# Optimization experiments

Measured on AMD Instinct MI355X. Metric: run time of the kernel, lower is better.

## Reference

```python
import jax, jax.numpy as jnp
import numpy as np

B, C, H, W = 16, 256, 56, 56
NH = 8           # num_heads
BS = 8           # block_size
HALO = 3         # halo_size
WIN = BS + 2 * HALO   # 14
MLP = 4


def setup_inputs() -> dict:
    key = jax.random.key(0)
    ks = jax.random.split(key, 8)
    f = lambda k, shape, s: jax.random.normal(k, shape, jnp.float32) * s
    return dict(
        x=jax.random.normal(ks[0], (B, C, H, W), jnp.float32),
        ln1_g=jnp.ones((C,), jnp.float32), ln1_b=jnp.zeros((C,), jnp.float32),
        wq=f(ks[1], (C, C), C ** -0.5), bq=jnp.zeros((C,), jnp.float32),
        wkv=f(ks[2], (2 * C, C), C ** -0.5), bkv=jnp.zeros((2 * C,), jnp.float32),
        bias=f(ks[3], (1, NH, 1, BS * BS, WIN * WIN), 0.02),
        gamma1=jnp.full((1, C, 1, 1), 1e-6, jnp.float32),
        ln2_g=jnp.ones((C,), jnp.float32), ln2_b=jnp.zeros((C,), jnp.float32),
        w1=f(ks[4], (MLP * C, C), 0.02), b1=jnp.zeros((MLP * C,), jnp.float32),
        w2=f(ks[5], (C, MLP * C), 0.02), b2=jnp.zeros((C,), jnp.float32),
        gamma2=jnp.full((1, 1, 1, C), 1e-6, jnp.float32),
    )


def _ln2d(x, g, b, eps=1e-5):
    # LayerNorm over channel dim of NCHW
    mu = jnp.mean(x, axis=1, keepdims=True)
    var = jnp.mean((x - mu) ** 2, axis=1, keepdims=True)
    return (x - mu) * jax.lax.rsqrt(var + eps) * g[None, :, None, None] + b[None, :, None, None]


def _halo_attn(x, wq, bq, wkv, bkv, bias):
    Bn, Cc, Hh, Ww = x.shape
    dh = Cc // NH
    scale = dh ** -0.5
    nHb, nWb = Hh // BS, Ww // BS
    xh = jnp.transpose(x, (0, 2, 3, 1))            # B,H,W,C
    q = xh @ wq.T + bq                             # 1x1 conv
    kv = xh @ wkv.T + bkv                          # B,H,W,2C
    # q blocks: B,nh,nblocks,bs^2,dh
    q = q.reshape(Bn, nHb, BS, nWb, BS, NH, dh).transpose(0, 5, 1, 3, 2, 4, 6)
    q = q.reshape(Bn, NH, nHb * nWb, BS * BS, dh)
    # kv halo windows
    kvp = jnp.pad(kv, ((0, 0), (HALO, HALO), (HALO, HALO), (0, 0)))
    ih = (jnp.arange(nHb) * BS)[:, None] + jnp.arange(WIN)[None, :]
    iw = (jnp.arange(nWb) * BS)[:, None] + jnp.arange(WIN)[None, :]
    kvw = kvp[:, ih[:, None, :, None], iw[None, :, None, :], :]
    kvw = kvw.reshape(Bn, nHb * nWb, WIN * WIN, NH, 2 * dh).transpose(0, 3, 1, 2, 4)
    k, v = kvw[..., :dh], kvw[..., dh:]
    attn = jnp.einsum('bhnqd,bhnkd->bhnqk', q, k) * scale + bias
    attn = jax.nn.softmax(attn, axis=-1)
    out = jnp.einsum('bhnqk,bhnkd->bhnqd', attn, v)                   # B,nh,nb,bs^2,dh
    out = out.reshape(Bn, NH, nHb, nWb, BS, BS, dh).transpose(0, 1, 6, 2, 4, 3, 5)
    return out.reshape(Bn, Cc, Hh, Ww)


def _forward(x, ln1_g, ln1_b, wq, bq, wkv, bkv, bias, gamma1,
             ln2_g, ln2_b, w1, b1, w2, b2, gamma2):
    shortcut = x
    a = _halo_attn(_ln2d(x, ln1_g, ln1_b), wq, bq, wkv, bkv, bias)
    x = shortcut + gamma1 * a
    shortcut = x
    y = jnp.transpose(_ln2d(x, ln2_g, ln2_b), (0, 2, 3, 1))           # NHWC
    y = jax.nn.gelu(y @ w1.T + b1, approximate=False) @ w2.T + b2
    y = gamma2 * y
    return shortcut + jnp.transpose(y, (0, 3, 1, 2))


def reference(x, ln1_g, ln1_b, wq, bq, wkv, bkv, bias, gamma1,
              ln2_g, ln2_b, w1, b1, w2, b2, gamma2):
    return _forward(x, ln1_g, ln1_b, wq, bq, wkv, bkv, bias, gamma1,
                    ln2_g, ln2_b, w1, b1, w2, b2, gamma2)
```

## Files before the change

### kernel.cpp

```cpp
#include <hip/hip_runtime.h>
#include <hip/hip_bf16.h>
#include <math.h>

typedef unsigned short u16;
typedef float f32x4 __attribute__((ext_vector_type(4)));
typedef __bf16 bf16x8 __attribute__((ext_vector_type(8)));

__device__ __forceinline__ float bf2f(u16 u) {
    union { float f; unsigned int i; } v; v.i = ((unsigned int)u) << 16; return v.f;
}
__device__ __forceinline__ u16 f2bf(float f) {
    union { float f; unsigned int i; } v; v.f = f;
    unsigned int x = v.i;
    return (u16)((x + 0x7FFFu + ((x >> 16) & 1u)) >> 16);
}
__device__ __forceinline__ unsigned int cvt_pk_bf16(float lo, float hi) {
    unsigned int r;
    asm("v_cvt_pk_bf16_f32 %0, %1, %2" : "=v"(r) : "v"(lo), "v"(hi));
    return r;
}

__global__ __launch_bounds__(256) void k_prep(const float* __restrict__ wq, const float* __restrict__ wkv,
                                              const float* __restrict__ w1, const float* __restrict__ w2,
                                              u16* __restrict__ wqkvb, u16* __restrict__ w1p, u16* __restrict__ w2p) {
    const int bid = blockIdx.x, t = threadIdx.x;
    if (bid < 192) {
        int e = (bid * 256 + t) * 4;
        const float* src = (e < 65536) ? (wq + e) : (wkv + (e - 65536));
        float sc = (e < 65536) ? 0.17677669529663687f : 1.f;
        float4 v = *(const float4*)src;
        ushort4 o;
        o.x = f2bf(v.x * sc); o.y = f2bf(v.y * sc); o.z = f2bf(v.z * sc); o.w = f2bf(v.w * sc);
        *(ushort4*)(wqkvb + e) = o;
    } else if (bid < 320) {
        int tid = (bid - 192) * 256 + t;
        int kc = tid >> 11, rem = tid & 2047;
        int wave = rem >> 9, rem2 = rem & 511;
        int ks = rem2 >> 6, lane = rem2 & 63;
        int ln = lane & 15, quad = lane >> 4;
        const float* src = w1 + (size_t)(kc * 64 + wave * 16 + ln) * 256 + ks * 32 + quad * 8;
        float4 v0 = *(const float4*)src;
        float4 v1 = *(const float4*)(src + 4);
        alignas(16) u16 tmp[8];
        tmp[0] = f2bf(v0.x); tmp[1] = f2bf(v0.y); tmp[2] = f2bf(v0.z); tmp[3] = f2bf(v0.w);
        tmp[4] = f2bf(v1.x); tmp[5] = f2bf(v1.y); tmp[6] = f2bf(v1.z); tmp[7] = f2bf(v1.w);
        *(int4*)(w1p + (size_t)tid * 8) = *(int4*)tmp;
    } else {
        int tid = (bid - 320) * 256 + t;
        int kc = tid >> 11, rem = tid & 2047;
        int wave = rem >> 9, rem2 = rem & 511;
        int ks2 = rem2 >> 8, rem3 = rem2 & 255;
        int nt = rem3 >> 6, lane = rem3 & 63;
        int ln = lane & 15, quad = lane >> 4;
        const float* src = w2 + (size_t)(wave * 64 + nt * 16 + ln) * 1024 + kc * 64 + ks2 * 32 + quad * 8;
        float4 v0 = *(const float4*)src;
        float4 v1 = *(const float4*)(src + 4);
        alignas(16) u16 tmp[8];
        tmp[0] = f2bf(v0.x); tmp[1] = f2bf(v0.y); tmp[2] = f2bf(v0.z); tmp[3] = f2bf(v0.w);
        tmp[4] = f2bf(v1.x); tmp[5] = f2bf(v1.y); tmp[6] = f2bf(v1.z); tmp[7] = f2bf(v1.w);
        *(int4*)(w2p + (size_t)tid * 8) = *(int4*)tmp;
    }
}

__global__ __launch_bounds__(256) void k_transpose(const float* __restrict__ x, u16* __restrict__ xh) {
    __shared__ __align__(16) u16 tile[64][72];
    const int t = threadIdx.x;
    const int hw0 = blockIdx.x * 64;
    const int c0  = blockIdx.y * 64;
    const int b   = blockIdx.z;
    const int cl = t >> 2, wl = (t & 3) * 16;
    {
        int c = c0 + cl;
        const float* src = x + (size_t)(b * 256 + c) * 3136 + hw0 + wl;
        for (int q = 0; q < 4; q++) {
            float4 v = *(const float4*)(src + q * 4);
            uint2 pr;
            pr.x = cvt_pk_bf16(v.x, v.y);
            pr.y = cvt_pk_bf16(v.z, v.w);
            *(uint2*)&tile[cl][wl + q * 4] = pr;
        }
    }
    __syncthreads();
    const int hl = t >> 3, cl2 = (t & 7) * 8;
    for (int i = 0; i < 2; i++) {
        int hw = hl + i * 32;
        alignas(16) u16 tmp[8];
        for (int j = 0; j < 8; j++) tmp[j] = tile[cl2 + j][hw];
        u16* dst = xh + (size_t)(b * 3136 + hw0 + hw) * 256 + c0 + cl2;
        *(int4*)dst = *(int4*)tmp;
    }
}

__global__ __launch_bounds__(256) void k_ln(const u16* __restrict__ in, u16* __restrict__ out,
                                            const float* __restrict__ g, const float* __restrict__ bta) {
    const int wave = threadIdx.x >> 6, lane = threadIdx.x & 63;
    const int p = blockIdx.x * 4 + wave;
    ushort4 v = *(const ushort4*)(in + (size_t)p * 256 + lane * 4);
    float f0 = bf2f(v.x), f1 = bf2f(v.y), f2 = bf2f(v.z), f3 = bf2f(v.w);
    float s = f0 + f1 + f2 + f3;
    float sq = f0 * f0 + f1 * f1 + f2 * f2 + f3 * f3;
    for (int o = 32; o >= 1; o >>= 1) { s += __shfl_xor(s, o, 64); sq += __shfl_xor(sq, o, 64); }
    float m = s * (1.f / 256.f);
    float var = sq * (1.f / 256.f) - m * m;
    float inv = rsqrtf(var + 1e-5f);
    float4 gv = *(const float4*)(g + lane * 4);
    float4 bv = *(const float4*)(bta + lane * 4);
    uint2 o2;
    o2.x = cvt_pk_bf16((f0 - m) * inv * gv.x + bv.x, (f1 - m) * inv * gv.y + bv.y);
    o2.y = cvt_pk_bf16((f2 - m) * inv * gv.z + bv.z, (f3 - m) * inv * gv.w + bv.w);
    *(uint2*)(out + (size_t)p * 256 + lane * 4) = o2;
}

__global__ __launch_bounds__(256) void k_qkv(
    const u16* __restrict__ xn, const u16* __restrict__ Bw,
    const float* __restrict__ bq, const float* __restrict__ bkv,
    u16* __restrict__ out) {
    __shared__ __align__(16) u16 smem[17408];
    u16* As = smem;
    u16* Bs = smem + 4096;

    const int g = blockIdx.x;
    const int xcd = g & 7, idx = g >> 3;
    const int bm = xcd * 49 + idx / 6, bn = idx % 6;

    const int t = threadIdx.x;
    const int wave = t >> 6, lane = t & 63;
    const int wm = (wave >> 1) * 64, wn = (wave & 1) * 64;
    const int ln = lane & 15, quad = lane >> 4;

    f32x4 vzero = {0.f, 0.f, 0.f, 0.f};
    f32x4 acc[4][4];
    for (int i = 0; i < 4; i++) for (int j = 0; j < 4; j++) acc[i][j] = vzero;

    const int srow = t >> 2;
    const int scol = (t & 3) * 8;

    for (int k0 = 0; k0 < 256; k0 += 32) {
        for (int i = 0; i < 2; i++) {
            int r = srow + i * 64;
            *(int4*)&As[r * 32 + scol] = *(const int4*)(xn + (size_t)(bm * 128 + r) * 256 + k0 + scol);
            *(int4*)&Bs[r * 32 + scol] = *(const int4*)(Bw + (size_t)(bn * 128 + r) * 256 + k0 + scol);
        }
        __syncthreads();
        bf16x8 af[4], bfr[4];
        for (int mt = 0; mt < 4; mt++) af[mt] = *(const bf16x8*)&As[(wm + mt * 16 + ln) * 32 + quad * 8];
        for (int nt = 0; nt < 4; nt++) bfr[nt] = *(const bf16x8*)&Bs[(wn + nt * 16 + ln) * 32 + quad * 8];
        for (int mt = 0; mt < 4; mt++)
            for (int nt = 0; nt < 4; nt++)
                acc[mt][nt] = __builtin_amdgcn_mfma_f32_16x16x32_bf16(bfr[nt], af[mt], acc[mt][nt], 0, 0, 0);
        __syncthreads();
    }

    u16* Cs = smem;
    for (int nt = 0; nt < 4; nt++) {
        int gn0 = bn * 128 + wn + nt * 16 + quad * 4;
        f32x4 bv;
        if (gn0 < 256) {
            f32x4 tq = *(const f32x4*)(bq + gn0);
            bv = tq * 0.17677669529663687f;
        } else {
            bv = *(const f32x4*)(bkv + gn0 - 256);
        }
        for (int mt = 0; mt < 4; mt++) {
            uint2 pk2;
            pk2.x = cvt_pk_bf16(acc[mt][nt][0] + bv[0], acc[mt][nt][1] + bv[1]);
            pk2.y = cvt_pk_bf16(acc[mt][nt][2] + bv[2], acc[mt][nt][3] + bv[3]);
            *(uint2*)&Cs[(wm + mt * 16 + ln) * 136 + wn + nt * 16 + quad * 4] = pk2;
        }
    }
    __syncthreads();
    const int row = t >> 4, col = (t & 15) * 8;
    for (int pass = 0; pass < 8; pass++) {
        int rr = pass * 16 + row;
        int4 v = *(int4*)&Cs[rr * 136 + col];
        *(int4*)(out + (size_t)(bm * 128 + rr) * 768 + bn * 128 + col) = v;
    }
}

__global__ __launch_bounds__(256) void k_mlp(
    const u16* __restrict__ xn, const u16* __restrict__ x2,
    const u16* __restrict__ w1p, const float* __restrict__ b1,
    const u16* __restrict__ w2p, const float* __restrict__ b2,
    const float* __restrict__ g2v, float* __restrict__ outT) {
    __shared__ __align__(16) u16 smem[16896 + 8704];
    u16* As = smem;
    u16* Hs = smem + 16896;

    const int g = blockIdx.x;
    const int bm = (g & 7) * 98 + (g >> 3);

    const int t = threadIdx.x;
    const int wave = t >> 6, lane = t & 63;
    const int ln = lane & 15, quad = lane >> 4;
    const int wn64 = wave * 64;
    const int wq4 = wave * 2;

    f32x4 vzero = {0.f, 0.f, 0.f, 0.f};
    f32x4 acc[4][4];
    for (int i = 0; i < 4; i++) for (int j = 0; j < 4; j++) acc[i][j] = vzero;

    {
        const int srow = t >> 2, scb = (t & 3) * 8;
        for (int c = 0; c < 8; c++) {
            int col = scb + c * 32;
            *(int4*)&As[srow * 264 + col] = *(const int4*)(xn + (size_t)(bm * 64 + srow) * 256 + col);
        }
    }
    __syncthreads();

    for (int kc = 0; kc < 8; kc++) {
        bf16x8 w1f[2][8];
        {
            const u16* w1b = w1p + (size_t)(kc * 8 + wq4) * 4096 + lane * 8;
            #pragma unroll
            for (int nt = 0; nt < 2; nt++)
                #pragma unroll
                for (int ks = 0; ks < 8; ks++)
                    w1f[nt][ks] = *(const bf16x8*)(w1b + nt * 4096 + ks * 512);
        }
        f32x4 up[4][2];
        #pragma unroll
        for (int i = 0; i < 4; i++) { up[i][0] = vzero; up[i][1] = vzero; }
        #pragma unroll
        for (int ks = 0; ks < 8; ks++) {
            #pragma unroll
            for (int mt = 0; mt < 4; mt++) {
                bf16x8 af = *(const bf16x8*)&As[(mt * 16 + ln) * 264 + ks * 32 + quad * 8];
                up[mt][0] = __builtin_amdgcn_mfma_f32_16x16x32_bf16(w1f[0][ks], af, up[mt][0], 0, 0, 0);
                up[mt][1] = __builtin_amdgcn_mfma_f32_16x16x32_bf16(w1f[1][ks], af, up[mt][1], 0, 0, 0);
            }
        }
        bf16x8 w2f[4][4];
        #pragma unroll
        for (int ks2 = 0; ks2 < 4; ks2++) {
            const u16* w2b = w2p + (size_t)((((kc * 2 + (ks2 >> 1)) * 4 + wave) * 2 + (ks2 & 1)) * 4) * 512 + lane * 8;
            #pragma unroll
            for (int nt = 0; nt < 4; nt++)
                w2f[ks2][nt] = *(const bf16x8*)(w2b + nt * 512);
        }
        __syncthreads();
        #pragma unroll
        for (int nt = 0; nt < 2; nt++) {
            float4 bv = *(const float4*)(b1 + kc * 128 + wave * 32 + nt * 16 + quad * 4);
            #pragma unroll
            for (int mt = 0; mt < 4; mt++) {
                float v0 = up[mt][nt][0] + bv.x;
                float v1 = up[mt][nt][1] + bv.y;
                float v2 = up[mt][nt][2] + bv.z;
                float v3 = up[mt][nt][3] + bv.w;
                uint2 pk;
                pk.x = cvt_pk_bf16(v0 * (1.f / (1.f + __expf(-1.702f * v0))),
                                   v1 * (1.f / (1.f + __expf(-1.702f * v1))));
                pk.y = cvt_pk_bf16(v2 * (1.f / (1.f + __expf(-1.702f * v2))),
                                   v3 * (1.f / (1.f + __expf(-1.702f * v3))));
                *(uint2*)&Hs[(mt * 16 + ln) * 136 + wave * 32 + nt * 16 + quad * 4] = pk;
            }
        }
        __syncthreads();
        #pragma unroll
        for (int ks2 = 0; ks2 < 4; ks2++) {
            bf16x8 hf[4];
            #pragma unroll
            for (int mt = 0; mt < 4; mt++)
                hf[mt] = *(const bf16x8*)&Hs[(mt * 16 + ln) * 136 + ks2 * 32 + quad * 8];
            #pragma unroll
            for (int nt = 0; nt < 4; nt++) {
                #pragma unroll
                for (int mt = 0; mt < 4; mt++)
                    acc[mt][nt] = __builtin_amdgcn_mfma_f32_16x16x32_bf16(hf[mt], w2f[ks2][nt], acc[mt][nt], 0, 0, 0);
            }
        }
    }

    const int b = bm / 49;
    for (int nt = 0; nt < 4; nt++) {
        int gn = wn64 + nt * 16 + ln;
        float bs = b2[gn], g2 = g2v[gn];
        for (int mt = 0; mt < 4; mt++) {
            int gm0 = bm * 64 + mt * 16 + quad * 4;
            int hw0 = gm0 - b * 3136;
            f32x4 res;
            for (int r = 0; r < 4; r++)
                res[r] = bf2f(x2[(size_t)(gm0 + r) * 256 + gn]) + g2 * (acc[mt][nt][r] + bs);
            *(f32x4*)(outT + (size_t)(b * 256 + gn) * 3136 + hw0) = res;
        }
    }
}

__global__ __launch_bounds__(256, 4) void k_attn(
    const u16* __restrict__ qkv, const float* __restrict__ bias,
    const u16* __restrict__ xh, const float* __restrict__ gamma1,
    u16* __restrict__ x2) {
    __shared__ __align__(16) u16 Kl[208 * 40];
    __shared__ __align__(16) u16 Vt[32 * 236];

    const int t = threadIdx.x;
    const int blk = blockIdx.x, head = blockIdx.y, b = blockIdx.z;
    const int bh = blk / 7, bw = blk - bh * 7;
    const int wave = t >> 6, lane = t & 63;
    const int ln = lane & 15, quad = lane >> 4;

    for (int cid = t; cid < 208 * 8; cid += 256) {
        int pos = cid >> 3, part = cid & 7;
        int i = pos / 14, j = pos - i * 14;
        int gh = bh * 8 - 3 + i, gw = bw * 8 - 3 + j;
        bool valid = (pos < 196) && ((unsigned)gh < 56u) && ((unsigned)gw < 56u);
        int d0 = (part & 3) * 8;
        int4 v = {0, 0, 0, 0};
        if (valid) {
            size_t p = (size_t)(b * 56 + gh) * 56 + gw;
            v = *(const int4*)(qkv + p * 768 + 256 + head * 64 + ((part & 4) ? 32 : 0) + d0);
        }
        if (!(part & 4)) {
            *(int4*)&Kl[pos * 40 + d0] = v;
        } else {
            alignas(16) u16 tmp[8];
            *(int4*)tmp = v;
            for (int jj = 0; jj < 8; jj++) Vt[(d0 + jj) * 236 + pos] = tmp[jj];
        }
    }
    __syncthreads();

    const int qrow = wave * 16 + ln;
    const int qh = bh * 8 + (qrow >> 3), qw = bw * 8 + (qrow & 7);
    const size_t qp = (size_t)(b * 56 + qh) * 56 + qw;
    bf16x8 qf = *(const bf16x8*)(qkv + qp * 768 + head * 32 + quad * 8);

    f32x4 s[13];
    const float* bp = bias + (size_t)(head * 64 + qrow) * 196 + quad * 4;
    #pragma unroll
    for (int nt = 0; nt < 13; nt++) {
        bf16x8 kf = *(const bf16x8*)&Kl[(nt * 16 + ln) * 40 + quad * 8];
        f32x4 c;
        if (nt < 12 || quad == 0) {
            c = *(const f32x4*)(bp + nt * 16);
        } else {
            c = (f32x4){-1e30f, -1e30f, -1e30f, -1e30f};
        }
        s[nt] = __builtin_amdgcn_mfma_f32_16x16x32_bf16(kf, qf, c, 0, 0, 0);
    }

    float mx = -1e30f;
    #pragma unroll
    for (int nt = 0; nt < 13; nt++)
        #pragma unroll
        for (int r = 0; r < 4; r++) mx = fmaxf(mx, s[nt][r]);
    mx = fmaxf(mx, __shfl_xor(mx, 16, 64));
    mx = fmaxf(mx, __shfl_xor(mx, 32, 64));
    float sum = 0.f;
    #pragma unroll
    for (int nt = 0; nt < 13; nt++)
        #pragma unroll
        for (int r = 0; r < 4; r++) {
            float e = __expf(s[nt][r] - mx);
            s[nt][r] = e;
            sum += e;
        }
    sum += __shfl_xor(sum, 16, 64);
    sum += __shfl_xor(sum, 32, 64);
    float rinv = 1.f / sum;

    unsigned int pk[13][2];
    #pragma unroll
    for (int nt = 0; nt < 13; nt++) {
        pk[nt][0] = cvt_pk_bf16(s[nt][0], s[nt][1]);
        pk[nt][1] = cvt_pk_bf16(s[nt][2], s[nt][3]);
    }

    f32x4 vzero = {0.f, 0.f, 0.f, 0.f};
    f32x4 o_acc[2];
    o_acc[0] = vzero; o_acc[1] = vzero;
    #pragma unroll
    for (int kc = 0; kc < 7; kc++) {
        union { int4 i4; bf16x8 v; } pu;
        pu.i4.x = pk[2 * kc][0];
        pu.i4.y = pk[2 * kc][1];
        pu.i4.z = (kc < 6) ? pk[2 * kc + 1][0] : 0;
        pu.i4.w = (kc < 6) ? pk[2 * kc + 1][1] : 0;
        #pragma unroll
        for (int n2 = 0; n2 < 2; n2++) {
            union { int4 i4; bf16x8 v; } vu;
            const u16* vb = &Vt[(n2 * 16 + ln) * 236 + kc * 32 + quad * 4];
            *(int2*)&vu.i4.x = *(const int2*)vb;
            if (kc < 6) {
                *(int2*)&vu.i4.z = *(const int2*)(vb + 16);
            } else {
                vu.i4.z = 0; vu.i4.w = 0;
            }
            o_acc[n2] = __builtin_amdgcn_mfma_f32_16x16x32_bf16(pu.v, vu.v, o_acc[n2], 0, 0, 0);
        }
    }

    float rr4[4];
    #pragma unroll
    for (int r = 0; r < 4; r++) rr4[r] = __shfl(rinv, quad * 4 + r, 16);

    #pragma unroll
    for (int n2 = 0; n2 < 2; n2++) {
        int c = head * 32 + n2 * 16 + ln;
        float g1 = gamma1[c];
        #pragma unroll
        for (int r = 0; r < 4; r++) {
            int q = wave * 16 + quad * 4 + r;
            int hh = bh * 8 + (q >> 3), ww = bw * 8 + (q & 7);
            size_t p = (size_t)(b * 56 + hh) * 56 + ww;
            float a = o_acc[n2][r] * rr4[r];
            x2[p * 256 + c] = f2bf(bf2f(xh[p * 256 + c]) + g1 * a);
        }
    }
}

extern "C" void kernel_launch(void* const* d_in, const int* in_sizes, int n_in,
                              void* d_out, int out_size, void* d_ws, size_t ws_size,
                              hipStream_t stream) {
    const float* x      = (const float*)d_in[0];
    const float* ln1_g  = (const float*)d_in[1];
    const float* ln1_b  = (const float*)d_in[2];
    const float* wq     = (const float*)d_in[3];
    const float* bq     = (const float*)d_in[4];
    const float* wkv    = (const float*)d_in[5];
    const float* bkv    = (const float*)d_in[6];
    const float* bias   = (const float*)d_in[7];
    const float* gamma1 = (const float*)d_in[8];
    const float* ln2_g  = (const float*)d_in[9];
    const float* ln2_b  = (const float*)d_in[10];
    const float* w1     = (const float*)d_in[11];
    const float* b1     = (const float*)d_in[12];
    const float* w2     = (const float*)d_in[13];
    const float* b2     = (const float*)d_in[14];
    const float* gamma2 = (const float*)d_in[15];

    char* ws = (char*)d_ws;
    u16* qkv   = (u16*)ws;
    u16* xh    = (u16*)(ws + 77070336);
    u16* x2    = (u16*)(ws + 102760448);
    u16* wqkvb = (u16*)(ws + 128450560);
    u16* w1p   = (u16*)(ws + 128843776);
    u16* w2p   = (u16*)(ws + 129368064);
    u16* xn1   = x2;
    u16* xn2   = xh;

    k_prep<<<dim3(448), 256, 0, stream>>>(wq, wkv, w1, w2, wqkvb, w1p, w2p);
    k_transpose<<<dim3(49, 4, 16), 256, 0, stream>>>(x, xh);
    k_ln<<<dim3(12544), 256, 0, stream>>>(xh, xn1, ln1_g, ln1_b);
    k_qkv<<<dim3(2352), 256, 0, stream>>>(xn1, wqkvb, bq, bkv, qkv);
    k_attn<<<dim3(49, 8, 16), 256, 0, stream>>>(qkv, bias, xh, gamma1, x2);
    k_ln<<<dim3(12544), 256, 0, stream>>>(x2, xn2, ln2_g, ln2_b);
    k_mlp<<<dim3(784), 256, 0, stream>>>(xn2, x2, w1p, b1, w2p, b2, gamma2, (float*)d_out);
}
```

Measured before the change: 335.5 us.

## Fuse second LayerNorm into attention epilogue stats and MLP prologue

The attention kernel now reduces per-head partial sums and sums of squares of the residual output and writes them to a small stats buffer. The MLP kernel combines these partials into mean and variance and applies LayerNorm while staging its input tile, so the standalone k_ln launch and its read and write of a full activation tensor go away. The cost is extra shuffles in the attention epilogue and per-row normalization work in the MLP prologue. Variance is now computed as E[x^2]-m^2, which is less numerically stable than the two-pass form.

```diff
diff --git a/kernel.cpp b/kernel.cpp
--- a/kernel.cpp
+++ b/kernel.cpp
@@ -178,10 +178,12 @@
 }
 
 __global__ __launch_bounds__(256) void k_mlp(
-    const u16* __restrict__ xn, const u16* __restrict__ x2,
+    const u16* __restrict__ x2,
     const u16* __restrict__ w1p, const float* __restrict__ b1,
     const u16* __restrict__ w2p, const float* __restrict__ b2,
-    const float* __restrict__ g2v, float* __restrict__ outT) {
+    const float* __restrict__ g2v,
+    const float* __restrict__ ln2g, const float* __restrict__ ln2b,
+    const float* __restrict__ ln2s, float* __restrict__ outT) {
     __shared__ __align__(16) u16 smem[16896 + 8704];
     u16* As = smem;
     u16* Hs = smem + 16896;
@@ -201,9 +203,37 @@
 
     {
         const int srow = t >> 2, scb = (t & 3) * 8;
+        const size_t prow = (size_t)(bm * 64 + srow);
+        const float4* stp = (const float4*)(ln2s + prow * 16);
+        float4 s0 = stp[0], s1 = stp[1], s2 = stp[2], s3 = stp[3];
+        float S = s0.x + s0.z + s1.x + s1.z + s2.x + s2.z + s3.x + s3.z;
+        float Q = s0.y + s0.w + s1.y + s1.w + s2.y + s2.w + s3.y + s3.w;
+        float m = S * (1.f / 256.f);
+        float var = Q * (1.f / 256.f) - m * m;
+        float inv = rsqrtf(var + 1e-5f);
+        const u16* src = x2 + prow * 256;
+        #pragma unroll
         for (int c = 0; c < 8; c++) {
             int col = scb + c * 32;
-            *(int4*)&As[srow * 264 + col] = *(const int4*)(xn + (size_t)(bm * 64 + srow) * 256 + col);
+            int4 raw = *(const int4*)(src + col);
+            float4 g0 = *(const float4*)(ln2g + col);
+            float4 g1 = *(const float4*)(ln2g + col + 4);
+            float4 b0 = *(const float4*)(ln2b + col);
+            float4 b1v = *(const float4*)(ln2b + col + 4);
+            const unsigned int* u = (const unsigned int*)&raw;
+            float f[8];
+            #pragma unroll
+            for (int k = 0; k < 4; k++) {
+                union { unsigned int i; float f; } lo, hi;
+                lo.i = u[k] << 16; hi.i = u[k] & 0xFFFF0000u;
+                f[2 * k] = lo.f; f[2 * k + 1] = hi.f;
+            }
+            uint4 o;
+            o.x = cvt_pk_bf16((f[0] - m) * inv * g0.x + b0.x, (f[1] - m) * inv * g0.y + b0.y);
+            o.y = cvt_pk_bf16((f[2] - m) * inv * g0.z + b0.z, (f[3] - m) * inv * g0.w + b0.w);
+            o.z = cvt_pk_bf16((f[4] - m) * inv * g1.x + b1v.x, (f[5] - m) * inv * g1.y + b1v.y);
+            o.w = cvt_pk_bf16((f[6] - m) * inv * g1.z + b1v.z, (f[7] - m) * inv * g1.w + b1v.w);
+            *(uint4*)&As[srow * 264 + col] = o;
         }
     }
     __syncthreads();
@@ -290,7 +320,7 @@
 __global__ __launch_bounds__(256, 4) void k_attn(
     const u16* __restrict__ qkv, const float* __restrict__ bias,
     const u16* __restrict__ xh, const float* __restrict__ gamma1,
-    u16* __restrict__ x2) {
+    u16* __restrict__ x2, float* __restrict__ ln2s) {
     __shared__ __align__(16) u16 Kl[208 * 40];
     __shared__ __align__(16) u16 Vt[32 * 236];
 
@@ -395,6 +425,8 @@
     #pragma unroll
     for (int r = 0; r < 4; r++) rr4[r] = __shfl(rinv, quad * 4 + r, 16);
 
+    float sacc[4] = {0.f, 0.f, 0.f, 0.f};
+    float qacc[4] = {0.f, 0.f, 0.f, 0.f};
     #pragma unroll
     for (int n2 = 0; n2 < 2; n2++) {
         int c = head * 32 + n2 * 16 + ln;
@@ -405,7 +437,29 @@
             int hh = bh * 8 + (q >> 3), ww = bw * 8 + (q & 7);
             size_t p = (size_t)(b * 56 + hh) * 56 + ww;
             float a = o_acc[n2][r] * rr4[r];
-            x2[p * 256 + c] = f2bf(bf2f(xh[p * 256 + c]) + g1 * a);
+            u16 u = f2bf(bf2f(xh[p * 256 + c]) + g1 * a);
+            x2[p * 256 + c] = u;
+            float vq = bf2f(u);
+            sacc[r] += vq;
+            qacc[r] += vq * vq;
+        }
+    }
+    #pragma unroll
+    for (int r = 0; r < 4; r++) {
+        #pragma unroll
+        for (int o = 1; o < 16; o <<= 1) {
+            sacc[r] += __shfl_xor(sacc[r], o, 16);
+            qacc[r] += __shfl_xor(qacc[r], o, 16);
+        }
+    }
+    if (ln == 0) {
+        #pragma unroll
+        for (int r = 0; r < 4; r++) {
+            int q = wave * 16 + quad * 4 + r;
+            int hh = bh * 8 + (q >> 3), ww = bw * 8 + (q & 7);
+            size_t p = (size_t)(b * 56 + hh) * 56 + ww;
+            float2 st; st.x = sacc[r]; st.y = qacc[r];
+            *(float2*)(ln2s + p * 16 + head * 2) = st;
         }
     }
 }
@@ -431,20 +485,19 @@
     const float* gamma2 = (const float*)d_in[15];
 
     char* ws = (char*)d_ws;
-    u16* qkv   = (u16*)ws;
-    u16* xh    = (u16*)(ws + 77070336);
-    u16* x2    = (u16*)(ws + 102760448);
-    u16* wqkvb = (u16*)(ws + 128450560);
-    u16* w1p   = (u16*)(ws + 128843776);
-    u16* w2p   = (u16*)(ws + 129368064);
-    u16* xn1   = x2;
-    u16* xn2   = xh;
+    u16*   qkv   = (u16*)ws;
+    u16*   xh    = (u16*)(ws + 77070336);
+    u16*   x2    = (u16*)(ws + 102760448);
+    u16*   wqkvb = (u16*)(ws + 128450560);
+    u16*   w1p   = (u16*)(ws + 128843776);
+    u16*   w2p   = (u16*)(ws + 129368064);
+    float* ln2s  = (float*)(ws + 129892352);
+    u16*   xn1   = x2;
 
     k_prep<<<dim3(448), 256, 0, stream>>>(wq, wkv, w1, w2, wqkvb, w1p, w2p);
     k_transpose<<<dim3(49, 4, 16), 256, 0, stream>>>(x, xh);
     k_ln<<<dim3(12544), 256, 0, stream>>>(xh, xn1, ln1_g, ln1_b);
     k_qkv<<<dim3(2352), 256, 0, stream>>>(xn1, wqkvb, bq, bkv, qkv);
-    k_attn<<<dim3(49, 8, 16), 256, 0, stream>>>(qkv, bias, xh, gamma1, x2);
-    k_ln<<<dim3(12544), 256, 0, stream>>>(x2, xn2, ln2_g, ln2_b);
-    k_mlp<<<dim3(784), 256, 0, stream>>>(xn2, x2, w1p, b1, w2p, b2, gamma2, (float*)d_out);
-}
+    k_attn<<<dim3(49, 8, 16), 256, 0, stream>>>(qkv, bias, xh, gamma1, x2, ln2s);
+    k_mlp<<<dim3(784), 256, 0, stream>>>(x2, w1p, b1, w2p, b2, gamma2, ln2_g, ln2_b, ln2s, (float*)d_out);
+}
```

Result: no change. 336.1 us (+0.2%).
